# Kernel optimization log

Measured on AMD Instinct MI355X. Metric: run time of the kernel, lower is better.

Reference implementation:

```python
import jax, jax.numpy as jnp
import numpy as np

K = 3          # conv kernel size
G = 3          # KAN grid intervals
SPLINE_K = 3   # B-spline order
N_BASIS = G + SPLINE_K  # 6


def extended_grid():
    # pykan-style grid on [-1, 1] with G intervals, extended by k knots each side
    h = 2.0 / G
    return jnp.arange(-SPLINE_K, G + SPLINE_K + 1, dtype=jnp.float32) * h - 1.0  # [G+2k+1]


def bspline_basis(x, t, k):
    """Cox-de Boor recursion. x: [...], t: [m] knots -> [..., m-1-k] bases."""
    x = x[..., None]
    b = ((x >= t[:-1]) & (x < t[1:])).astype(x.dtype)  # degree 0: [..., m-1]
    for d in range(1, k + 1):
        left = (x - t[: -(d + 1)]) / (t[d:-1] - t[: -(d + 1)]) * b[..., :-1]
        right = (t[d + 1:] - x) / (t[d + 1:] - t[1:-d]) * b[..., 1:]
        b = left + right
    return b  # [..., m-1-k]


def setup_inputs() -> dict:
    key = jax.random.key(0)
    k1, k2, k3, k4 = jax.random.split(key, 4)
    B, C, H, W = 32, 16, 64, 64
    in_dim, out_dim = C * K * K, 64
    x = jax.random.normal(k1, (B, C, H, W), dtype=jnp.float32)
    coef = jax.random.normal(k2, (in_dim, out_dim, N_BASIS), dtype=jnp.float32) * 0.1
    scale_base = jax.random.normal(k3, (in_dim, out_dim), dtype=jnp.float32) * (1.0 / np.sqrt(in_dim))
    scale_sp = jnp.ones((in_dim, out_dim), dtype=jnp.float32) + 0.0 * jax.random.normal(k4, (in_dim, out_dim))
    return {"x": x, "coef": coef, "scale_base": scale_base, "scale_sp": scale_sp}


def reference(x, coef, scale_base, scale_sp):
    B, C, H, W = x.shape
    Ho, Wo = H - K + 1, W - K + 1
    # im2col with torch-reshape ordering: feature index = c*K*K + di*K + dj
    cols = [x[:, :, di:di + Ho, dj:dj + Wo] for di in range(K) for dj in range(K)]
    patches = jnp.stack(cols, axis=2)                    # [B, C, K*K, Ho, Wo]
    patches = patches.reshape(B, C * K * K, Ho, Wo)      # [B, D, Ho, Wo]
    p = patches.transpose(0, 2, 3, 1)                    # [B, Ho, Wo, D]

    t = extended_grid()
    basis = bspline_basis(p, t, SPLINE_K)                # [B, Ho, Wo, D, N_BASIS]
    # spline part: sum over input dims and bases, with per-edge scale_sp folded into coef
    spline = jnp.einsum('bhwdn,don->bhwo', basis, coef * scale_sp[:, :, None])
    base = jnp.einsum('bhwd,do->bhwo', jax.nn.silu(p), scale_base)
    y = base + spline                                    # [B, Ho, Wo, O]
    return y.transpose(0, 3, 1, 2)                       # [B, O, Ho, Wo]
```

## Files before the change

### kernel.cpp

```cpp
#include <hip/hip_runtime.h>
#include <math.h>

#define Bsz 32
#define Cc  16
#define Hh  64
#define Ww  64
#define HO  62
#define WO  62
#define OD  64
#define ND  144
#define TILE_U4 (2048 + 16)

using short8 = __attribute__((ext_vector_type(8))) short;
using f32x4  = __attribute__((ext_vector_type(4))) float;
using f32x16 = __attribute__((ext_vector_type(16))) float;
typedef unsigned int u32;
typedef unsigned short ushort;

__device__ __forceinline__ ushort f2bf(float f) {
    union { float f; unsigned u; } v; v.f = f;
    unsigned r = v.u + 0x7fff + ((v.u >> 16) & 1);
    return (ushort)(r >> 16);
}
__device__ __forceinline__ float bf2f(ushort h) {
    union { unsigned u; float f; } v; v.u = ((unsigned)h) << 16; return v.f;
}

__device__ __forceinline__ uint4 feat_pack(float xv) {
    float xi = (xv + 3.0f) * 1.5f;
    float fi = floorf(xi);
    int   ii = (int)fi;
    float u  = xi - fi;
    float u2 = u * u, u3 = u2 * u;
    float P0 = u3 * (1.0f / 6.0f);
    float P1 = (1.0f + 3.0f * u + 3.0f * u2 - 3.0f * u3) * (1.0f / 6.0f);
    float P2 = (4.0f - 6.0f * u2 + 3.0f * u3) * (1.0f / 6.0f);
    float om = 1.0f - u;
    float P3 = om * om * om * (1.0f / 6.0f);
    bool ok = (ii >= 0) && (ii <= 8);
    float bas[6];
    #pragma unroll
    for (int n = 0; n < 6; ++n) {
        int t = ii - n;
        float v = (t == 0) ? P0 : (t == 1) ? P1 : (t == 2) ? P2 : (t == 3) ? P3 : 0.0f;
        bas[n] = ok ? v : 0.0f;
    }
    float s = xv / (1.0f + __expf(-xv));
    ushort sh = f2bf(s);
    ushort sl = f2bf(s - bf2f(sh));
    uint4 pk;
    pk.x = (unsigned)f2bf(bas[0]) | ((unsigned)f2bf(bas[1]) << 16);
    pk.y = (unsigned)f2bf(bas[2]) | ((unsigned)f2bf(bas[3]) << 16);
    pk.z = (unsigned)f2bf(bas[4]) | ((unsigned)f2bf(bas[5]) << 16);
    pk.w = (unsigned)sh | ((unsigned)sl << 16);
    return pk;
}

__global__ __launch_bounds__(256) void kan_prep6(const float* __restrict__ coef,
                                                 const float* __restrict__ sbase,
                                                 const float* __restrict__ ssp,
                                                 ushort* __restrict__ wpb) {
    int g = blockIdx.x * 256 + threadIdx.x;
    if (g >= ND * 64) return;
    int n = g & 63, slot = g >> 6;
    int pass = slot / 72, r72 = slot - pass * 72;
    int t = r72 >> 1, par = r72 & 1;
    int a = t / 9, rem = t - a * 9;
    int c = pass * 8 + 2 * a + par;
    int d = c * 9 + rem;
    float sspv = ssp[d * OD + n];
    ushort sb = f2bf(sbase[d * OD + n]);
    ushort v[8];
    #pragma unroll
    for (int f = 0; f < 6; ++f) v[f] = f2bf(coef[(d * OD + n) * 6 + f] * sspv);
    v[6] = sb; v[7] = sb;
    uint4 pk;
    pk.x = (unsigned)v[0] | ((unsigned)v[1] << 16);
    pk.y = (unsigned)v[2] | ((unsigned)v[3] << 16);
    pk.z = (unsigned)v[4] | ((unsigned)v[5] << 16);
    pk.w = (unsigned)v[6] | ((unsigned)v[7] << 16);
    *(uint4*)&wpb[(size_t)g * 8] = pk;
}

__global__ __launch_bounds__(256, 4) void kan_fused3(const float* __restrict__ x,
                                                     const uint4* __restrict__ wpb,
                                                     float* __restrict__ out) {
    __shared__ uint4 feat[TILE_U4];

    const int tid  = threadIdx.x;
    const int wid  = tid >> 6;
    const int lane = tid & 63;
    const int l31  = lane & 31;
    const int hi   = lane >> 5;
    const int mt   = blockIdx.x;
    const int bb   = blockIdx.y;
    const int h0   = mt * 2;

    f32x16 acc0, acc1;
    #pragma unroll
    for (int i = 0; i < 16; ++i) { acc0[i] = 0.0f; acc1[i] = 0.0f; }

    const int m0 = wid * 32 + l31;
    const int hh = m0 >> 6, w = m0 & 63;
    const short8* abase = (const short8*)feat + (hi * 256 + hh * 64 + w);
    const int fr = tid >> 6, fw = tid & 63;

    #pragma unroll 1
    for (int pass = 0; pass < 2; ++pass) {
        if (pass) __syncthreads();
        #pragma unroll 1
        for (int j = 0; j < 8; ++j) {
            float xv = x[(size_t)bb * 65536 + (size_t)(pass * 8 + j) * 4096 + (h0 + fr) * 64 + fw];
            feat[j * 256 + tid] = feat_pack(xv);
        }
        __syncthreads();

        const uint4* bp = wpb + (size_t)(pass * 72) * 64 + hi * 64 + l31;
        short8 pb0 = *(const short8*)bp;
        short8 pb1 = *(const short8*)(bp + 32);

        #pragma unroll 1
        for (int a = 0; a < 4; ++a) {
            const short8* ap = abase + a * 512;
            #pragma unroll
            for (int rem = 0; rem < 9; ++rem) {
                const int di = rem / 3, dj = rem - di * 3;
                short8 b0 = pb0, b1 = pb1;
                bp += 128;
                pb0 = *(const short8*)bp;
                pb1 = *(const short8*)(bp + 32);
                short8 av = ap[di * 64 + dj];
                acc0 = __builtin_amdgcn_mfma_f32_32x32x16_bf16(av, b0, acc0, 0, 0, 0);
                acc1 = __builtin_amdgcn_mfma_f32_32x32x16_bf16(av, b1, acc1, 0, 0, 0);
            }
        }
    }

    float* Csc = (float*)feat;
    __syncthreads();
    {
        #pragma unroll
        for (int r = 0; r < 16; ++r) {
            int ml = (r & 3) + ((r >> 2) << 3) + (hi << 2);
            Csc[(size_t)l31 * 130 + wid * 32 + ml] = acc0[r];
        }
        __syncthreads();
        #pragma unroll
        for (int it = 0; it < 8; ++it) {
            int flat = it * 256 + tid;
            int o = flat >> 6, hh2 = (flat >> 5) & 1, fc = flat & 31;
            if (fc < 31) {
                float2 v = *(float2*)&Csc[(size_t)o * 130 + hh2 * 64 + fc * 2];
                *(float2*)&out[((size_t)(bb * OD + o) * HO + h0 + hh2) * WO + fc * 2] = v;
            }
        }
    }
    __syncthreads();
    {
        #pragma unroll
        for (int r = 0; r < 16; ++r) {
            int ml = (r & 3) + ((r >> 2) << 3) + (hi << 2);
            Csc[(size_t)l31 * 130 + wid * 32 + ml] = acc1[r];
        }
        __syncthreads();
        #pragma unroll
        for (int it = 0; it < 8; ++it) {
            int flat = it * 256 + tid;
            int o = flat >> 6, hh2 = (flat >> 5) & 1, fc = flat & 31;
            if (fc < 31) {
                float2 v = *(float2*)&Csc[(size_t)o * 130 + hh2 * 64 + fc * 2];
                *(float2*)&out[((size_t)(bb * OD + 32 + o) * HO + h0 + hh2) * WO + fc * 2] = v;
            }
        }
    }
}

__global__ __launch_bounds__(256, 4) void kan_diag(float* __restrict__ dst) {
    const int tid = threadIdx.x;
    short v = (short)(tid + 1);
    short8 av = {v, v, v, v, v, v, v, v};
    short8 b0 = {1, 2, 3, 4, 5, 6, 7, 8};
    short8 b1 = {8, 7, 6, 5, 4, 3, 2, 1};
    f32x16 acc0, acc1;
    #pragma unroll
    for (int i = 0; i < 16; ++i) { acc0[i] = 0.0f; acc1[i] = 0.0f; }
    #pragma unroll 1
    for (int t = 0; t < 72; ++t) {
        acc0 = __builtin_amdgcn_mfma_f32_32x32x16_bf16(av, b0, acc0, 0, 0, 0);
        acc1 = __builtin_amdgcn_mfma_f32_32x32x16_bf16(av, b1, acc1, 0, 0, 0);
    }
    size_t flat = ((size_t)blockIdx.y * 31 + blockIdx.x) * 256 + tid;
    f32x4 o = {acc0[0] + acc1[0], acc0[5] + acc1[5], acc0[10] + acc1[10], acc0[15] + acc1[15]};
    *(f32x4*)&dst[flat * 4] = o;
}

#define NCHUNK 36
#define FW 68
__global__ __launch_bounds__(256) void kan_prep(const float* __restrict__ coef,
                                                const float* __restrict__ sbase,
                                                const float* __restrict__ ssp,
                                                ushort* __restrict__ wp) {
    int idx = blockIdx.x * 256 + threadIdx.x;
    if (idx >= ND * OD * 8) return;
    int n = idx & 7, o = (idx >> 3) & 63, d = idx >> 9;
    float v = (n < 6) ? coef[(d * OD + o) * 6 + n] * ssp[d * OD + o] : sbase[d * OD + o];
    wp[idx] = f2bf(v);
}

__global__ __launch_bounds__(128) void kan_mfma(const float* __restrict__ x,
                                                const ushort* __restrict__ wp,
                                                float* __restrict__ out) {
    __shared__ uint4 feat[Cc * 4 * FW];
    const int rp = blockIdx.x, b = blockIdx.y, tid = threadIdx.x;
    const int wid = tid >> 6, lane = tid & 63, l15 = lane & 15, ks = lane >> 4;
    const int hrow0 = rp * 2;
    for (int i = tid; i < Cc * 4 * FW; i += 128) {
        int wl = i % FW, cr = i / FW, r = cr & 3, c = cr >> 2;
        int col = wl < Ww ? wl : Ww - 1;
        feat[i] = feat_pack(x[((b * Cc + c) * Hh + hrow0 + r) * Ww + col]);
    }
    __syncthreads();
    f32x4 acc[4][4];
    #pragma unroll
    for (int rt = 0; rt < 4; ++rt)
        #pragma unroll
        for (int ct = 0; ct < 4; ++ct) acc[rt][ct] = (f32x4){0.f, 0.f, 0.f, 0.f};
    auto loadA = [&](int chunk, short8* A) {
        int d = chunk * 4 + ks;
        int c = (d * 57) >> 9;
        int rem = d - c * 9;
        int di = (rem * 11) >> 5;
        int dj = rem - di * 3;
        const short8* ap = (const short8*)&feat[(c * 4 + wid + di) * FW + l15 + dj];
        A[0] = ap[0]; A[1] = ap[16]; A[2] = ap[32]; A[3] = ap[48];
    };
    auto loadB = [&](int chunk, short8* Bf) {
        int d = chunk * 4 + ks;
        const short8* bp = (const short8*)wp + (d * 64 + l15);
        Bf[0] = bp[0]; Bf[1] = bp[16]; Bf[2] = bp[32]; Bf[3] = bp[48];
    };
    short8 A0[4], B0[4], A1[4], B1[4];
    loadA(0, A0); loadB(0, B0);
    for (int cb = 0; cb < NCHUNK; cb += 2) {
        loadA(cb + 1, A1); loadB(cb + 1, B1);
        #pragma unroll
        for (int rt = 0; rt < 4; ++rt)
            #pragma unroll
            for (int ct = 0; ct < 4; ++ct)
                acc[rt][ct] = __builtin_amdgcn_mfma_f32_16x16x32_bf16(A0[rt], B0[ct], acc[rt][ct], 0, 0, 0);
        if (cb + 2 < NCHUNK) { loadA(cb + 2, A0); loadB(cb + 2, B0); }
        #pragma unroll
        for (int rt = 0; rt < 4; ++rt)
            #pragma unroll
            for (int ct = 0; ct < 4; ++ct)
                acc[rt][ct] = __builtin_amdgcn_mfma_f32_16x16x32_bf16(A1[rt], B1[ct], acc[rt][ct], 0, 0, 0);
    }
    __syncthreads();
    float* sC = ((float*)feat) + wid * (OD * FW);
    #pragma unroll
    for (int rt = 0; rt < 4; ++rt)
        #pragma unroll
        for (int ct = 0; ct < 4; ++ct)
            *(f32x4*)&sC[(ct * 16 + l15) * FW + rt * 16 + ks * 4] = acc[rt][ct];
    const int orow = hrow0 + wid;
    for (int j = 0; j < OD; ++j) {
        float v = sC[j * FW + lane];
        if (lane < WO) out[((b * OD + j) * HO + orow) * WO + lane] = v;
    }
}

extern "C" void kernel_launch(void* const* d_in, const int* in_sizes, int n_in,
                              void* d_out, int out_size, void* d_ws, size_t ws_size,
                              hipStream_t stream) {
    (void)in_sizes; (void)n_in; (void)out_size;
    const float* x     = (const float*)d_in[0];
    const float* coef  = (const float*)d_in[1];
    const float* sbase = (const float*)d_in[2];
    const float* ssp   = (const float*)d_in[3];
    float* out = (float*)d_out;

    const size_t wpb_bytes = (size_t)ND * 64 * 16;

    if (ws_size >= wpb_bytes + 4096) {
        uint4* wpb = (uint4*)d_ws;
        kan_prep6<<<36, 256, 0, stream>>>(coef, sbase, ssp, (ushort*)wpb);
        if (ws_size >= (8u << 20)) {
            float* diag = (float*)((char*)d_ws + (1u << 20));
            dim3 gridd(31, Bsz);
            kan_diag<<<gridd, 256, 0, stream>>>(diag);
        }
        dim3 grid(31, Bsz);
        kan_fused3<<<grid, 256, 0, stream>>>(x, wpb, out);
    } else if (ws_size >= (size_t)ND * OD * 8 * 2) {
        ushort* wp = (ushort*)d_ws;
        kan_prep<<<(ND * OD * 8 + 255) / 256, 256, 0, stream>>>(coef, sbase, ssp, wp);
        dim3 grid(HO / 2, Bsz);
        kan_mfma<<<grid, 128, 0, stream>>>(x, wp, out);
    }
}
```

Baseline: 59.03 us.

## Stage weight tiles into LDS via global_load_lds and drop diagnostic kernel

The fused KAN conv kernel now copies each chunk of 18 packed bf16 weight rows into shared memory with async global-to-LDS loads, then reads the B operands from LDS instead of prefetching them per-lane from global memory. It also removes the kan_diag MFMA probe kernel that previously ran before the main kernel whenever the workspace was large. Occupancy hint drops from 4 to 3 blocks per CU because of the larger LDS footprint, and extra __syncthreads are added around each weight chunk load.

```diff
diff --git a/kernel.cpp b/kernel.cpp
--- a/kernel.cpp
+++ b/kernel.cpp
@@ -9,7 +9,8 @@
 #define WO  62
 #define OD  64
 #define ND  144
-#define TILE_U4 (2048 + 16)
+#define FEAT_U4 2064
+#define BSM_U4  1152
 
 using short8 = __attribute__((ext_vector_type(8))) short;
 using f32x4  = __attribute__((ext_vector_type(4))) float;
@@ -24,6 +25,12 @@
 }
 __device__ __forceinline__ float bf2f(ushort h) {
     union { unsigned u; float f; } v; v.u = ((unsigned)h) << 16; return v.f;
+}
+
+__device__ __forceinline__ void gload_lds16(const void* g, void* l) {
+    __builtin_amdgcn_global_load_lds((const __attribute__((address_space(1))) u32*)g,
+                                     (__attribute__((address_space(3))) u32*)l,
+                                     16, 0, 0);
 }
 
 __device__ __forceinline__ uint4 feat_pack(float xv) {
@@ -82,10 +89,12 @@
     *(uint4*)&wpb[(size_t)g * 8] = pk;
 }
 
-__global__ __launch_bounds__(256, 4) void kan_fused3(const float* __restrict__ x,
+__global__ __launch_bounds__(256, 3) void kan_fused4(const float* __restrict__ x,
                                                      const uint4* __restrict__ wpb,
                                                      float* __restrict__ out) {
-    __shared__ uint4 feat[TILE_U4];
+    __shared__ uint4 smem[FEAT_U4 + BSM_U4];
+    uint4* feat = smem;
+    char*  bsmB = (char*)(smem + FEAT_U4);
 
     const int tid  = threadIdx.x;
     const int wid  = tid >> 6;
@@ -103,6 +112,7 @@
     const int m0 = wid * 32 + l31;
     const int hh = m0 >> 6, w = m0 & 63;
     const short8* abase = (const short8*)feat + (hi * 256 + hh * 64 + w);
+    const short8* bbase = (const short8*)bsmB + (hi * 64 + l31);
     const int fr = tid >> 6, fw = tid & 63;
 
     #pragma unroll 1
@@ -113,23 +123,29 @@
             float xv = x[(size_t)bb * 65536 + (size_t)(pass * 8 + j) * 4096 + (h0 + fr) * 64 + fw];
             feat[j * 256 + tid] = feat_pack(xv);
         }
-        __syncthreads();
-
-        const uint4* bp = wpb + (size_t)(pass * 72) * 64 + hi * 64 + l31;
-        short8 pb0 = *(const short8*)bp;
-        short8 pb1 = *(const short8*)(bp + 32);
 
         #pragma unroll 1
         for (int a = 0; a < 4; ++a) {
+            __syncthreads();
+            const char* src = (const char*)wpb + ((size_t)(pass * 72 + a * 18) * 64) * 16;
+            #pragma unroll
+            for (int q = 0; q < 4; ++q) {
+                int ch = q * 4 + wid;
+                gload_lds16(src + (size_t)(ch * 64 + lane) * 16, bsmB + ch * 1024);
+            }
+            if (wid < 2) {
+                int ch = 16 + wid;
+                gload_lds16(src + (size_t)(ch * 64 + lane) * 16, bsmB + ch * 1024);
+            }
+            __syncthreads();
+
             const short8* ap = abase + a * 512;
             #pragma unroll
             for (int rem = 0; rem < 9; ++rem) {
                 const int di = rem / 3, dj = rem - di * 3;
-                short8 b0 = pb0, b1 = pb1;
-                bp += 128;
-                pb0 = *(const short8*)bp;
-                pb1 = *(const short8*)(bp + 32);
                 short8 av = ap[di * 64 + dj];
+                short8 b0 = bbase[rem * 128];
+                short8 b1 = bbase[rem * 128 + 32];
                 acc0 = __builtin_amdgcn_mfma_f32_32x32x16_bf16(av, b0, acc0, 0, 0, 0);
                 acc1 = __builtin_amdgcn_mfma_f32_32x32x16_bf16(av, b1, acc1, 0, 0, 0);
             }
@@ -173,25 +189,6 @@
             }
         }
     }
-}
-
-__global__ __launch_bounds__(256, 4) void kan_diag(float* __restrict__ dst) {
-    const int tid = threadIdx.x;
-    short v = (short)(tid + 1);
-    short8 av = {v, v, v, v, v, v, v, v};
-    short8 b0 = {1, 2, 3, 4, 5, 6, 7, 8};
-    short8 b1 = {8, 7, 6, 5, 4, 3, 2, 1};
-    f32x16 acc0, acc1;
-    #pragma unroll
-    for (int i = 0; i < 16; ++i) { acc0[i] = 0.0f; acc1[i] = 0.0f; }
-    #pragma unroll 1
-    for (int t = 0; t < 72; ++t) {
-        acc0 = __builtin_amdgcn_mfma_f32_32x32x16_bf16(av, b0, acc0, 0, 0, 0);
-        acc1 = __builtin_amdgcn_mfma_f32_32x32x16_bf16(av, b1, acc1, 0, 0, 0);
-    }
-    size_t flat = ((size_t)blockIdx.y * 31 + blockIdx.x) * 256 + tid;
-    f32x4 o = {acc0[0] + acc1[0], acc0[5] + acc1[5], acc0[10] + acc1[10], acc0[15] + acc1[15]};
-    *(f32x4*)&dst[flat * 4] = o;
 }
 
 #define NCHUNK 36
@@ -284,13 +281,8 @@
     if (ws_size >= wpb_bytes + 4096) {
         uint4* wpb = (uint4*)d_ws;
         kan_prep6<<<36, 256, 0, stream>>>(coef, sbase, ssp, (ushort*)wpb);
-        if (ws_size >= (8u << 20)) {
-            float* diag = (float*)((char*)d_ws + (1u << 20));
-            dim3 gridd(31, Bsz);
-            kan_diag<<<gridd, 256, 0, stream>>>(diag);
-        }
         dim3 grid(31, Bsz);
-        kan_fused3<<<grid, 256, 0, stream>>>(x, wpb, out);
+        kan_fused4<<<grid, 256, 0, stream>>>(x, wpb, out);
     } else if (ws_size >= (size_t)ND * OD * 8 * 2) {
         ushort* wp = (ushort*)d_ws;
         kan_prep<<<(ND * OD * 8 + 255) / 256, 256, 0, stream>>>(coef, sbase, ssp, wp);
```

New measurement: 63.73 us. 1.08x slower.
